# Optimization experiments

Measured on AMD Instinct MI355X. Metric: run time of the kernel, lower is better.

The kernel has to match this reference:

```python
import jax, jax.numpy as jnp
import numpy as np

N_SRC0, N_DST0 = 200000, 50000
N_DST1 = 10000
D_IN, D_HID = 128, 128


def _sage_mean(h, src, dst, n_dst, W_self, b_self, W_neigh, b_neigh, act):
    # gather messages from src nodes, mean-aggregate per dst node
    msg = h[src]                                             # [E, D]
    agg = jax.ops.segment_sum(msg, dst, num_segments=n_dst)  # [n_dst, D]
    deg = jax.ops.segment_sum(jnp.ones(dst.shape, h.dtype), dst, num_segments=n_dst)
    h_neigh = agg / jnp.maximum(deg, 1.0)[:, None]
    # DGL block convention: dst nodes are the first n_dst src nodes
    rst = h[:n_dst] @ W_self + b_self + h_neigh @ W_neigh + b_neigh
    return jax.nn.relu(rst) if act else rst


def setup_inputs() -> dict:
    key = jax.random.key(0)
    ks = jax.random.split(key, 12)
    s = 1.0 / np.sqrt(D_HID)
    return {
        "features": jax.random.normal(ks[0], (N_SRC0, D_IN), jnp.float32),
        "src0": jax.random.randint(ks[1], (800000,), 0, N_SRC0),
        "dst0": jax.random.randint(ks[2], (800000,), 0, N_DST0),
        "src1": jax.random.randint(ks[3], (160000,), 0, N_DST0),
        "dst1": jax.random.randint(ks[4], (160000,), 0, N_DST1),
        "W_init": jax.random.uniform(ks[5], (D_IN, D_HID), jnp.float32, -s, s),
        "b_init": jax.random.uniform(ks[6], (D_HID,), jnp.float32, -s, s),
        "W_self": jax.random.uniform(ks[7], (D_HID, D_HID), jnp.float32, -s, s),
        "b_self": jax.random.uniform(ks[8], (D_HID,), jnp.float32, -s, s),
        "W_neigh": jax.random.uniform(ks[9], (D_HID, D_HID), jnp.float32, -s, s),
        "b_neigh": jax.random.uniform(ks[10], (D_HID,), jnp.float32, -s, s),
    }


def reference(features, src0, dst0, src1, dst1, W_init, b_init, W_self, b_self, W_neigh, b_neigh):
    # fc_init + activation
    h = jax.nn.relu(features @ W_init + b_init)              # [N_SRC0, D_HID]
    # block 0 (act_flag True), dropout p=0.0 is identity
    h = _sage_mean(h, src0, dst0, N_DST0, W_self, b_self, W_neigh, b_neigh, act=True)
    # block 1 (last block: act_flag False)
    h = _sage_mean(h, src1, dst1, N_DST1, W_self, b_self, W_neigh, b_neigh, act=False)
    return jnp.squeeze(h, axis=1) if h.shape[1] == 1 else h  # h.squeeze(1) no-op for D_HID>1
```

## Files before the change

### kernel.cpp

```cpp
#include <hip/hip_runtime.h>
#include <stdint.h>
#include <stddef.h>


#define DIM 128
constexpr int N_SRC0 = 200000;
constexpr int N_DST0 = 50000;
constexpr int N_DST1 = 10000;
constexpr int E0 = 800000;
constexpr int E1 = 160000;
constexpr int MAXDEG = 64;

constexpr int FC_BLOCKS = 1024;
constexpr int PLACE_BLOCKS = 1024;

typedef __attribute__((ext_vector_type(8))) short bf16x8;
typedef __attribute__((ext_vector_type(4))) float f32x4;

__device__ __forceinline__ uint16_t f2bf(float f) {
  union { float f; uint32_t u; } v; v.f = f;
  return (uint16_t)((v.u + 0x7FFFu + ((v.u >> 16) & 1u)) >> 16);
}
__device__ __forceinline__ float bf2f(uint16_t h) {
  union { uint32_t u; float f; } v; v.u = ((uint32_t)h) << 16;
  return v.f;
}

__global__ __launch_bounds__(512) void prep_w_kernel(
    const float* __restrict__ W0, const float* __restrict__ W1,
    const float* __restrict__ W2, uint16_t* __restrict__ Wf,
    int* __restrict__ cnt, int ncnt) {
  int gid = blockIdx.x * 512 + threadIdx.x;
  if (gid < 3 * 16384) {
    int m = gid >> 14, idx = gid & 16383;
    const float* W = m == 0 ? W0 : (m == 1 ? W1 : W2);
    int j = idx & 7, lane = (idx >> 3) & 63, nt = (idx >> 9) & 7, kc = idx >> 12;
    int k = kc * 32 + (lane >> 4) * 8 + j;
    int n = nt * 16 + (lane & 15);
    Wf[gid] = f2bf(W[k * DIM + n]);
  }
  int z = gid - 3 * 16384;
  if (z >= 0 && z < ncnt) cnt[z] = 0;
}

__global__ __launch_bounds__(256, 4) void place_fc_kernel(
    const int* __restrict__ src0, const int* __restrict__ dst0,
    const int* __restrict__ src1, const int* __restrict__ dst1,
    int* __restrict__ cnt0, int* __restrict__ cnt1,
    int* __restrict__ eslot0, int* __restrict__ eslot1,
    const float* __restrict__ feat, const uint16_t* __restrict__ Wf,
    const float* __restrict__ bias, uint16_t* __restrict__ hout) {
  __shared__ __align__(16) float tile[2][4096];

  if ((blockIdx.x & 1) == 0) {
    int pb = blockIdx.x >> 1;
    int part = pb & 7;
    int bpp  = PLACE_BLOCKS >> 3;
    int bidx = pb >> 3;
    const int4* s04 = (const int4*)src0;
    const int4* d04 = (const int4*)dst0;
    const int4* s14 = (const int4*)src1;
    const int4* d14 = (const int4*)dst1;

    int lo = part * (N_DST0 / 8), hi = lo + (N_DST0 / 8);
    for (int i = bidx * 256 + threadIdx.x; i < E0 / 4; i += bpp * 256) {
      int4 d = d04[i]; int4 s = s04[i];
      if (d.x >= lo && d.x < hi) { int p = atomicAdd(&cnt0[d.x], 1); if (p < MAXDEG) eslot0[(size_t)d.x * MAXDEG + p] = s.x; }
      if (d.y >= lo && d.y < hi) { int p = atomicAdd(&cnt0[d.y], 1); if (p < MAXDEG) eslot0[(size_t)d.y * MAXDEG + p] = s.y; }
      if (d.z >= lo && d.z < hi) { int p = atomicAdd(&cnt0[d.z], 1); if (p < MAXDEG) eslot0[(size_t)d.z * MAXDEG + p] = s.z; }
      if (d.w >= lo && d.w < hi) { int p = atomicAdd(&cnt0[d.w], 1); if (p < MAXDEG) eslot0[(size_t)d.w * MAXDEG + p] = s.w; }
    }
    int lo1 = part * (N_DST1 / 8), hi1 = lo1 + (N_DST1 / 8);
    for (int i = bidx * 256 + threadIdx.x; i < E1 / 4; i += bpp * 256) {
      int4 d = d14[i]; int4 s = s14[i];
      if (d.x >= lo1 && d.x < hi1) { int p = atomicAdd(&cnt1[d.x], 1); if (p < MAXDEG) eslot1[(size_t)d.x * MAXDEG + p] = s.x; }
      if (d.y >= lo1 && d.y < hi1) { int p = atomicAdd(&cnt1[d.y], 1); if (p < MAXDEG) eslot1[(size_t)d.y * MAXDEG + p] = s.y; }
      if (d.z >= lo1 && d.z < hi1) { int p = atomicAdd(&cnt1[d.z], 1); if (p < MAXDEG) eslot1[(size_t)d.z * MAXDEG + p] = s.z; }
      if (d.w >= lo1 && d.w < hi1) { int p = atomicAdd(&cnt1[d.w], 1); if (p < MAXDEG) eslot1[(size_t)d.w * MAXDEG + p] = s.w; }
    }
    return;
  }

  const int tid = threadIdx.x;
  const int w = tid >> 6, lane = tid & 63;
  const int q = lane >> 4, m16 = lane & 15;
  const int sl = w >> 1, nh = w & 1;

  bf16x8 wv[4][4];
#pragma unroll
  for (int kc = 0; kc < 4; kc++)
#pragma unroll
    for (int j = 0; j < 4; j++)
      wv[kc][j] = *(const bf16x8*)&Wf[((size_t)((kc * 8 + nh * 4 + j) * 64 + lane)) * 8];

  float bv[4];
#pragma unroll
  for (int j = 0; j < 4; j++) bv[j] = bias[(nh * 4 + j) * 16 + m16];

  const int ntiles = N_SRC0 / 32;

  const int lrow0 = w * 8 + (lane >> 5);
  auto stage = [&](int t, int buf) {
#pragma unroll
    for (int i = 0; i < 4; i++) {
      int row = lrow0 + i * 2;
      int g = (lane & 31) ^ (row & 7);
      const float* gs = feat + (size_t)t * 4096 + row * 128 + g * 4;
      float* ld = &tile[buf][w * 1024 + i * 256];
      __builtin_amdgcn_global_load_lds(
          (const __attribute__((address_space(1))) uint32_t*)gs,
          (__attribute__((address_space(3))) uint32_t*)ld,
          16, 0, 0);
    }
  };

  int t = blockIdx.x >> 1;
  int cur = 0;
  if (t < ntiles) stage(t, 0);
  __syncthreads();

  const int trow = sl * 16 + m16;
  const int sw = trow & 7;

  while (t < ntiles) {
    int tn = t + FC_BLOCKS;
    if (tn < ntiles) stage(tn, cur ^ 1);

    f32x4 acc[4];
#pragma unroll
    for (int j = 0; j < 4; j++) acc[j] = (f32x4){0.f, 0.f, 0.f, 0.f};

    const char* rb = (const char*)&tile[cur][0] + trow * 512;
#pragma unroll
    for (int kc = 0; kc < 4; kc++) {
      int g0 = kc * 8 + q * 2;
      float4 x0 = *(const float4*)(rb + ((g0    ) ^ sw) * 16);
      float4 x1 = *(const float4*)(rb + ((g0 + 1) ^ sw) * 16);
      bf16x8 a;
      a[0] = (short)f2bf(x0.x); a[1] = (short)f2bf(x0.y);
      a[2] = (short)f2bf(x0.z); a[3] = (short)f2bf(x0.w);
      a[4] = (short)f2bf(x1.x); a[5] = (short)f2bf(x1.y);
      a[6] = (short)f2bf(x1.z); a[7] = (short)f2bf(x1.w);
#pragma unroll
      for (int j = 0; j < 4; j++)
        acc[j] = __builtin_amdgcn_mfma_f32_16x16x32_bf16(a, wv[kc][j], acc[j], 0, 0, 0);
    }

    int rowb = t * 32 + sl * 16 + q * 4;
#pragma unroll
    for (int j = 0; j < 4; j++)
#pragma unroll
      for (int r = 0; r < 4; r++) {
        float v = fmaxf(acc[j][r] + bv[j], 0.f);
        hout[(size_t)(rowb + r) * DIM + (nh * 4 + j) * 16 + m16] = f2bf(v);
      }

    __syncthreads();
    cur ^= 1;
    t = tn;
  }
}

__global__ __launch_bounds__(256) void agg_kernel(
    const int* __restrict__ eslot, const int* __restrict__ deg,
    const uint16_t* __restrict__ hsrc, uint16_t* __restrict__ hout, int n_dst) {
  int d = (blockIdx.x * 256 + threadIdx.x) >> 6;
  int lane = threadIdx.x & 63;
  if (d >= n_dst) return;
  const int* sl = eslot + (size_t)d * MAXDEG;
  int dg = deg[d];
  int dgc = dg < MAXDEG ? dg : MAXDEG;
  int qr = lane >> 4;
  int c  = lane & 15;

  float a0 = 0.f, a1 = 0.f, a2 = 0.f, a3 = 0.f;
  float a4 = 0.f, a5 = 0.f, a6 = 0.f, a7 = 0.f;

#define ACC4(P)                                                          \
  a0 += bf2f((uint16_t)(P).x); a1 += bf2f((uint16_t)((P).x >> 16));      \
  a2 += bf2f((uint16_t)(P).y); a3 += bf2f((uint16_t)((P).y >> 16));      \
  a4 += bf2f((uint16_t)(P).z); a5 += bf2f((uint16_t)((P).z >> 16));      \
  a6 += bf2f((uint16_t)(P).w); a7 += bf2f((uint16_t)((P).w >> 16));

  int e = 0;
  for (; e + 8 <= dgc; e += 8) {
    int s0 = sl[e + qr];
    int s1 = sl[e + 4 + qr];
    uint4 p0 = *(const uint4*)(hsrc + (size_t)s0 * DIM + c * 8);
    uint4 p1 = *(const uint4*)(hsrc + (size_t)s1 * DIM + c * 8);
    ACC4(p0); ACC4(p1);
  }
  for (; e + 4 <= dgc; e += 4) {
    int s0 = sl[e + qr];
    uint4 p0 = *(const uint4*)(hsrc + (size_t)s0 * DIM + c * 8);
    ACC4(p0);
  }
  int rem = dgc - e;
  if (qr < rem) {
    int s0 = sl[e + qr];
    uint4 p0 = *(const uint4*)(hsrc + (size_t)s0 * DIM + c * 8);
    ACC4(p0);
  }
#undef ACC4

  a0 += __shfl_xor(a0, 16); a0 += __shfl_xor(a0, 32);
  a1 += __shfl_xor(a1, 16); a1 += __shfl_xor(a1, 32);
  a2 += __shfl_xor(a2, 16); a2 += __shfl_xor(a2, 32);
  a3 += __shfl_xor(a3, 16); a3 += __shfl_xor(a3, 32);
  a4 += __shfl_xor(a4, 16); a4 += __shfl_xor(a4, 32);
  a5 += __shfl_xor(a5, 16); a5 += __shfl_xor(a5, 32);
  a6 += __shfl_xor(a6, 16); a6 += __shfl_xor(a6, 32);
  a7 += __shfl_xor(a7, 16); a7 += __shfl_xor(a7, 32);

  if (qr == 0) {
    float inv = 1.f / fmaxf((float)dg, 1.f);
    uint4 o;
    o.x = (uint32_t)f2bf(a0 * inv) | ((uint32_t)f2bf(a1 * inv) << 16);
    o.y = (uint32_t)f2bf(a2 * inv) | ((uint32_t)f2bf(a3 * inv) << 16);
    o.z = (uint32_t)f2bf(a4 * inv) | ((uint32_t)f2bf(a5 * inv) << 16);
    o.w = (uint32_t)f2bf(a6 * inv) | ((uint32_t)f2bf(a7 * inv) << 16);
    *(uint4*)(hout + (size_t)d * DIM + c * 8) = o;
  }
}

template <bool ACT, bool OUT_BF16>
__global__ __launch_bounds__(256) void sage_kernel(
    const uint16_t* __restrict__ hself, const uint16_t* __restrict__ hneigh,
    const uint16_t* __restrict__ WfS, const uint16_t* __restrict__ WfN,
    const float* __restrict__ bS, const float* __restrict__ bN,
    void* __restrict__ outp, int n_dst) {
  __shared__ uint16_t wS[16384];
  __shared__ uint16_t wN[16384];
  {
    const uint4* gS = (const uint4*)WfS;
    const uint4* gN = (const uint4*)WfN;
    uint4* sS = (uint4*)wS;
    uint4* sN = (uint4*)wN;
    for (int i = threadIdx.x; i < 2048; i += 256) { sS[i] = gS[i]; sN[i] = gN[i]; }
  }
  __syncthreads();

  int wave = (blockIdx.x * 256 + threadIdx.x) >> 6;
  int nwaves = (gridDim.x * 256) >> 6;
  int lane = threadIdx.x & 63;
  int q = lane >> 4, m16 = lane & 15;

  float bv[8];
#pragma unroll
  for (int nt = 0; nt < 8; nt++)
    bv[nt] = bS[nt * 16 + m16] + bN[nt * 16 + m16];

  const int nstrips = n_dst / 16;
  int s = wave;
  bf16x8 XS[4], XN[4];
  if (s < nstrips) {
    size_t ro = (size_t)(s * 16 + m16) * DIM + q * 8;
#pragma unroll
    for (int kc = 0; kc < 4; kc++) {
      XS[kc] = *(const bf16x8*)(hself + ro + kc * 32);
      XN[kc] = *(const bf16x8*)(hneigh + ro + kc * 32);
    }
  }

  while (s < nstrips) {
    int sn = s + nwaves;
    bf16x8 YS[4], YN[4];
    if (sn < nstrips) {
      size_t ro = (size_t)(sn * 16 + m16) * DIM + q * 8;
#pragma unroll
      for (int kc = 0; kc < 4; kc++) {
        YS[kc] = *(const bf16x8*)(hself + ro + kc * 32);
        YN[kc] = *(const bf16x8*)(hneigh + ro + kc * 32);
      }
    }

    f32x4 acc[8];
#pragma unroll
    for (int nt = 0; nt < 8; nt++) acc[nt] = (f32x4){0.f, 0.f, 0.f, 0.f};

#pragma unroll
    for (int kc = 0; kc < 4; kc++) {
#pragma unroll
      for (int nt = 0; nt < 8; nt++) {
        size_t fo = (size_t)((kc * 8 + nt) * 64 + lane) * 8;
        bf16x8 ws = *(const bf16x8*)&wS[fo];
        bf16x8 wn = *(const bf16x8*)&wN[fo];
        acc[nt] = __builtin_amdgcn_mfma_f32_16x16x32_bf16(XS[kc], ws, acc[nt], 0, 0, 0);
        acc[nt] = __builtin_amdgcn_mfma_f32_16x16x32_bf16(XN[kc], wn, acc[nt], 0, 0, 0);
      }
    }

    int m0 = s * 16;
#pragma unroll
    for (int nt = 0; nt < 8; nt++)
#pragma unroll
      for (int r = 0; r < 4; r++) {
        float v = acc[nt][r] + bv[nt];
        if (ACT) v = fmaxf(v, 0.f);
        size_t o = (size_t)(m0 + q * 4 + r) * DIM + nt * 16 + m16;
        if (OUT_BF16) ((uint16_t*)outp)[o] = f2bf(v);
        else          ((float*)outp)[o] = v;
      }

#pragma unroll
    for (int i = 0; i < 4; i++) { XS[i] = YS[i]; XN[i] = YN[i]; }
    s = sn;
  }
}

extern "C" void kernel_launch(void* const* d_in, const int* in_sizes, int n_in,
                              void* d_out, int out_size, void* d_ws, size_t ws_size,
                              hipStream_t stream) {
  const float* feat   = (const float*)d_in[0];
  const int* src0     = (const int*)d_in[1];
  const int* dst0     = (const int*)d_in[2];
  const int* src1     = (const int*)d_in[3];
  const int* dst1     = (const int*)d_in[4];
  const float* W_init = (const float*)d_in[5];
  const float* b_init = (const float*)d_in[6];
  const float* W_self = (const float*)d_in[7];
  const float* b_self = (const float*)d_in[8];
  const float* W_neigh= (const float*)d_in[9];
  const float* b_neigh= (const float*)d_in[10];

  char* ws = (char*)d_ws;
  uint16_t* h     = (uint16_t*)(ws + 0);
  uint16_t* h1    = (uint16_t*)(ws + 51200000);
  uint16_t* hn    = (uint16_t*)(ws + 64000000);
  int*      cnt0  = (int*)(ws + 76800000);
  int*      cnt1  = (int*)(ws + 77000000);
  int*      eslot0= (int*)(ws + 77040000);
  int*      eslot1= (int*)(ws + 89840000);
  uint16_t* WfI   = (uint16_t*)(ws + 92400000);
  uint16_t* WfS   = WfI + 16384;
  uint16_t* WfN   = WfS + 16384;

  prep_w_kernel<<<214, 512, 0, stream>>>(W_init, W_self, W_neigh, WfI, cnt0, 60000);

  place_fc_kernel<<<PLACE_BLOCKS + FC_BLOCKS, 256, 0, stream>>>(
      src0, dst0, src1, dst1, cnt0, cnt1, eslot0, eslot1,
      feat, WfI, b_init, h);

  agg_kernel<<<N_DST0 / 4, 256, 0, stream>>>(eslot0, cnt0, h, hn, N_DST0);
  sage_kernel<true, true><<<512, 256, 0, stream>>>(h, hn, WfS, WfN, b_self, b_neigh,
                                                   h1, N_DST0);

  agg_kernel<<<N_DST1 / 4, 256, 0, stream>>>(eslot1, cnt1, h1, hn, N_DST1);
  sage_kernel<false, false><<<160, 256, 0, stream>>>(h1, hn, WfS, WfN, b_self, b_neigh,
                                                     d_out, N_DST1);
}
```

Baseline: 270.6 us.

## Fold weight prep into fused kernels, drop LDS staging in fc_init, retune grids

Removes the separate prep_w kernel. W_init is now converted to bf16 MFMA layout in LDS by each fc block, W_self/W_neigh are converted by extra blocks in the first agg kernel, and counters are zeroed with hipMemsetAsync. The fc_init path now has each wave load a 16-row strip straight from global into registers, with no double-buffered LDS tiles, and computes all 8 N-tiles per wave. Place blocks are halved to a 1:2 ratio and the sage grid sizes change. Each fc block now repeats the W_init conversion, and the fc loads lose the async LDS prefetch.

```diff
diff --git a/kernel.cpp b/kernel.cpp
--- a/kernel.cpp
+++ b/kernel.cpp
@@ -11,8 +11,9 @@
 constexpr int E1 = 160000;
 constexpr int MAXDEG = 64;
 
+constexpr int PLACE_BLOCKS = 512;
 constexpr int FC_BLOCKS = 1024;
-constexpr int PLACE_BLOCKS = 1024;
+constexpr int PF_GRID = PLACE_BLOCKS + FC_BLOCKS;
 
 typedef __attribute__((ext_vector_type(8))) short bf16x8;
 typedef __attribute__((ext_vector_type(4))) float f32x4;
@@ -26,34 +27,17 @@
   return v.f;
 }
 
-__global__ __launch_bounds__(512) void prep_w_kernel(
-    const float* __restrict__ W0, const float* __restrict__ W1,
-    const float* __restrict__ W2, uint16_t* __restrict__ Wf,
-    int* __restrict__ cnt, int ncnt) {
-  int gid = blockIdx.x * 512 + threadIdx.x;
-  if (gid < 3 * 16384) {
-    int m = gid >> 14, idx = gid & 16383;
-    const float* W = m == 0 ? W0 : (m == 1 ? W1 : W2);
-    int j = idx & 7, lane = (idx >> 3) & 63, nt = (idx >> 9) & 7, kc = idx >> 12;
-    int k = kc * 32 + (lane >> 4) * 8 + j;
-    int n = nt * 16 + (lane & 15);
-    Wf[gid] = f2bf(W[k * DIM + n]);
-  }
-  int z = gid - 3 * 16384;
-  if (z >= 0 && z < ncnt) cnt[z] = 0;
-}
-
-__global__ __launch_bounds__(256, 4) void place_fc_kernel(
+__global__ __launch_bounds__(256) void place_fc_kernel(
     const int* __restrict__ src0, const int* __restrict__ dst0,
     const int* __restrict__ src1, const int* __restrict__ dst1,
     int* __restrict__ cnt0, int* __restrict__ cnt1,
     int* __restrict__ eslot0, int* __restrict__ eslot1,
-    const float* __restrict__ feat, const uint16_t* __restrict__ Wf,
+    const float* __restrict__ feat, const float* __restrict__ W_init,
     const float* __restrict__ bias, uint16_t* __restrict__ hout) {
-  __shared__ __align__(16) float tile[2][4096];
-
-  if ((blockIdx.x & 1) == 0) {
-    int pb = blockIdx.x >> 1;
+  __shared__ uint16_t wlds[16384];
+
+  if (blockIdx.x % 3 == 0) {
+    int pb = blockIdx.x / 3;
     int part = pb & 7;
     int bpp  = PLACE_BLOCKS >> 3;
     int bidx = pb >> 3;
@@ -81,89 +65,86 @@
     return;
   }
 
-  const int tid = threadIdx.x;
-  const int w = tid >> 6, lane = tid & 63;
+  for (int i = threadIdx.x; i < 16384; i += 256) {
+    int k = i >> 7, n = i & 127;
+    int off = (((k >> 5) * 8 + (n >> 4)) * 64 + ((k >> 3) & 3) * 16 + (n & 15)) * 8 + (k & 7);
+    wlds[off] = f2bf(W_init[i]);
+  }
+  __syncthreads();
+
+  int fcb = blockIdx.x - (blockIdx.x / 3 + 1);
+  const int lane = threadIdx.x & 63;
   const int q = lane >> 4, m16 = lane & 15;
-  const int sl = w >> 1, nh = w & 1;
-
-  bf16x8 wv[4][4];
-#pragma unroll
-  for (int kc = 0; kc < 4; kc++)
-#pragma unroll
-    for (int j = 0; j < 4; j++)
-      wv[kc][j] = *(const bf16x8*)&Wf[((size_t)((kc * 8 + nh * 4 + j) * 64 + lane)) * 8];
-
-  float bv[4];
-#pragma unroll
-  for (int j = 0; j < 4; j++) bv[j] = bias[(nh * 4 + j) * 16 + m16];
-
-  const int ntiles = N_SRC0 / 32;
-
-  const int lrow0 = w * 8 + (lane >> 5);
-  auto stage = [&](int t, int buf) {
-#pragma unroll
-    for (int i = 0; i < 4; i++) {
-      int row = lrow0 + i * 2;
-      int g = (lane & 31) ^ (row & 7);
-      const float* gs = feat + (size_t)t * 4096 + row * 128 + g * 4;
-      float* ld = &tile[buf][w * 1024 + i * 256];
-      __builtin_amdgcn_global_load_lds(
-          (const __attribute__((address_space(1))) uint32_t*)gs,
-          (__attribute__((address_space(3))) uint32_t*)ld,
-          16, 0, 0);
-    }
-  };
-
-  int t = blockIdx.x >> 1;
-  int cur = 0;
-  if (t < ntiles) stage(t, 0);
-  __syncthreads();
-
-  const int trow = sl * 16 + m16;
-  const int sw = trow & 7;
-
-  while (t < ntiles) {
-    int tn = t + FC_BLOCKS;
-    if (tn < ntiles) stage(tn, cur ^ 1);
-
-    f32x4 acc[4];
-#pragma unroll
-    for (int j = 0; j < 4; j++) acc[j] = (f32x4){0.f, 0.f, 0.f, 0.f};
-
-    const char* rb = (const char*)&tile[cur][0] + trow * 512;
+
+  float bv[8];
+#pragma unroll
+  for (int nt = 0; nt < 8; nt++) bv[nt] = bias[nt * 16 + m16];
+
+  const int nstrips = N_SRC0 / 16;
+  const int nw = FC_BLOCKS * 4;
+  int wave = fcb * 4 + (threadIdx.x >> 6);
+
+  for (int s = wave; s < nstrips; s += nw) {
+    const float* fr = feat + (size_t)(s * 16 + m16) * DIM + q * 8;
+    float4 x0[4], x1[4];
 #pragma unroll
     for (int kc = 0; kc < 4; kc++) {
-      int g0 = kc * 8 + q * 2;
-      float4 x0 = *(const float4*)(rb + ((g0    ) ^ sw) * 16);
-      float4 x1 = *(const float4*)(rb + ((g0 + 1) ^ sw) * 16);
-      bf16x8 a;
-      a[0] = (short)f2bf(x0.x); a[1] = (short)f2bf(x0.y);
-      a[2] = (short)f2bf(x0.z); a[3] = (short)f2bf(x0.w);
-      a[4] = (short)f2bf(x1.x); a[5] = (short)f2bf(x1.y);
-      a[6] = (short)f2bf(x1.z); a[7] = (short)f2bf(x1.w);
-#pragma unroll
-      for (int j = 0; j < 4; j++)
-        acc[j] = __builtin_amdgcn_mfma_f32_16x16x32_bf16(a, wv[kc][j], acc[j], 0, 0, 0);
-    }
-
-    int rowb = t * 32 + sl * 16 + q * 4;
-#pragma unroll
-    for (int j = 0; j < 4; j++)
+      x0[kc] = *(const float4*)(fr + kc * 32);
+      x1[kc] = *(const float4*)(fr + kc * 32 + 4);
+    }
+    bf16x8 a[4];
+#pragma unroll
+    for (int kc = 0; kc < 4; kc++) {
+      a[kc][0] = (short)f2bf(x0[kc].x); a[kc][1] = (short)f2bf(x0[kc].y);
+      a[kc][2] = (short)f2bf(x0[kc].z); a[kc][3] = (short)f2bf(x0[kc].w);
+      a[kc][4] = (short)f2bf(x1[kc].x); a[kc][5] = (short)f2bf(x1[kc].y);
+      a[kc][6] = (short)f2bf(x1[kc].z); a[kc][7] = (short)f2bf(x1[kc].w);
+    }
+
+    f32x4 acc[8];
+#pragma unroll
+    for (int nt = 0; nt < 8; nt++) acc[nt] = (f32x4){0.f, 0.f, 0.f, 0.f};
+
+#pragma unroll
+    for (int kc = 0; kc < 4; kc++)
+#pragma unroll
+      for (int nt = 0; nt < 8; nt++) {
+        bf16x8 wv = *(const bf16x8*)&wlds[((size_t)((kc * 8 + nt) * 64 + lane)) * 8];
+        acc[nt] = __builtin_amdgcn_mfma_f32_16x16x32_bf16(a[kc], wv, acc[nt], 0, 0, 0);
+      }
+
+    int rowb = s * 16 + q * 4;
+#pragma unroll
+    for (int nt = 0; nt < 8; nt++)
 #pragma unroll
       for (int r = 0; r < 4; r++) {
-        float v = fmaxf(acc[j][r] + bv[j], 0.f);
-        hout[(size_t)(rowb + r) * DIM + (nh * 4 + j) * 16 + m16] = f2bf(v);
-      }
-
-    __syncthreads();
-    cur ^= 1;
-    t = tn;
+        float v = fmaxf(acc[nt][r] + bv[nt], 0.f);
+        hout[(size_t)(rowb + r) * DIM + nt * 16 + m16] = f2bf(v);
+      }
   }
 }
 
 __global__ __launch_bounds__(256) void agg_kernel(
     const int* __restrict__ eslot, const int* __restrict__ deg,
-    const uint16_t* __restrict__ hsrc, uint16_t* __restrict__ hout, int n_dst) {
+    const uint16_t* __restrict__ hsrc, uint16_t* __restrict__ hout, int n_dst,
+    const float* __restrict__ WS_src, const float* __restrict__ WN_src,
+    uint16_t* __restrict__ Wf_out) {
+  int nagg = n_dst >> 2;
+  if (blockIdx.x >= nagg) {
+    int pid = (blockIdx.x - nagg) * 256 + threadIdx.x;
+#pragma unroll
+    for (int u = 0; u < 4; u++) {
+      int gid = pid * 4 + u;
+      int m = gid >> 14, idx = gid & 16383;
+      const float* W = m ? WN_src : WS_src;
+      int j = idx & 7, lane = (idx >> 3) & 63, nt = (idx >> 9) & 7, kc = idx >> 12;
+      int k = kc * 32 + (lane >> 4) * 8 + j;
+      int n = nt * 16 + (lane & 15);
+      Wf_out[gid] = f2bf(W[k * DIM + n]);
+    }
+    return;
+  }
+
   int d = (blockIdx.x * 256 + threadIdx.x) >> 6;
   int lane = threadIdx.x & 63;
   if (d >= n_dst) return;
@@ -335,17 +316,19 @@
   uint16_t* WfS   = WfI + 16384;
   uint16_t* WfN   = WfS + 16384;
 
-  prep_w_kernel<<<214, 512, 0, stream>>>(W_init, W_self, W_neigh, WfI, cnt0, 60000);
-
-  place_fc_kernel<<<PLACE_BLOCKS + FC_BLOCKS, 256, 0, stream>>>(
+  hipMemsetAsync(ws + 76800000, 0, 240000, stream);
+
+  place_fc_kernel<<<PF_GRID, 256, 0, stream>>>(
       src0, dst0, src1, dst1, cnt0, cnt1, eslot0, eslot1,
-      feat, WfI, b_init, h);
-
-  agg_kernel<<<N_DST0 / 4, 256, 0, stream>>>(eslot0, cnt0, h, hn, N_DST0);
-  sage_kernel<true, true><<<512, 256, 0, stream>>>(h, hn, WfS, WfN, b_self, b_neigh,
+      feat, W_init, b_init, h);
+
+  agg_kernel<<<N_DST0 / 4 + 32, 256, 0, stream>>>(eslot0, cnt0, h, hn, N_DST0,
+                                                  W_self, W_neigh, WfS);
+  sage_kernel<true, true><<<782, 256, 0, stream>>>(h, hn, WfS, WfN, b_self, b_neigh,
                                                    h1, N_DST0);
 
-  agg_kernel<<<N_DST1 / 4, 256, 0, stream>>>(eslot1, cnt1, h1, hn, N_DST1);
-  sage_kernel<false, false><<<160, 256, 0, stream>>>(h1, hn, WfS, WfN, b_self, b_neigh,
+  agg_kernel<<<N_DST1 / 4, 256, 0, stream>>>(eslot1, cnt1, h1, hn, N_DST1,
+                                             nullptr, nullptr, nullptr);
+  sage_kernel<false, false><<<157, 256, 0, stream>>>(h1, hn, WfS, WfN, b_self, b_neigh,
                                                      d_out, N_DST1);
 }
```

Result: slower. 335.0 us (+23.8%).

## Drop weight-prep kernel, convert weights inline, unroll gather, retune sage grids

Applied to the files above, without the earlier changes.

Removes the separate weight-prep kernel. Counters are now zeroed with hipMemsetAsync, the FC blocks convert W_init to bf16 directly from fp32 in registers, and the W_self/W_neigh swizzle is folded into 32 extra blocks of the first aggregation launch. The aggregation loop gains a 16-edge unrolled step for more memory-level parallelism, and the sage kernels' grid sizes change to 782 and 157 blocks. Each FC block now does strided scalar fp32 loads of W_init instead of vector loads of pre-swizzled bf16.

```diff
diff --git a/kernel.cpp b/kernel.cpp
--- a/kernel.cpp
+++ b/kernel.cpp
@@ -26,29 +26,12 @@
   return v.f;
 }
 
-__global__ __launch_bounds__(512) void prep_w_kernel(
-    const float* __restrict__ W0, const float* __restrict__ W1,
-    const float* __restrict__ W2, uint16_t* __restrict__ Wf,
-    int* __restrict__ cnt, int ncnt) {
-  int gid = blockIdx.x * 512 + threadIdx.x;
-  if (gid < 3 * 16384) {
-    int m = gid >> 14, idx = gid & 16383;
-    const float* W = m == 0 ? W0 : (m == 1 ? W1 : W2);
-    int j = idx & 7, lane = (idx >> 3) & 63, nt = (idx >> 9) & 7, kc = idx >> 12;
-    int k = kc * 32 + (lane >> 4) * 8 + j;
-    int n = nt * 16 + (lane & 15);
-    Wf[gid] = f2bf(W[k * DIM + n]);
-  }
-  int z = gid - 3 * 16384;
-  if (z >= 0 && z < ncnt) cnt[z] = 0;
-}
-
 __global__ __launch_bounds__(256, 4) void place_fc_kernel(
     const int* __restrict__ src0, const int* __restrict__ dst0,
     const int* __restrict__ src1, const int* __restrict__ dst1,
     int* __restrict__ cnt0, int* __restrict__ cnt1,
     int* __restrict__ eslot0, int* __restrict__ eslot1,
-    const float* __restrict__ feat, const uint16_t* __restrict__ Wf,
+    const float* __restrict__ feat, const float* __restrict__ W_init,
     const float* __restrict__ bias, uint16_t* __restrict__ hout) {
   __shared__ __align__(16) float tile[2][4096];
 
@@ -90,8 +73,11 @@
 #pragma unroll
   for (int kc = 0; kc < 4; kc++)
 #pragma unroll
-    for (int j = 0; j < 4; j++)
-      wv[kc][j] = *(const bf16x8*)&Wf[((size_t)((kc * 8 + nh * 4 + j) * 64 + lane)) * 8];
+    for (int jj = 0; jj < 4; jj++)
+#pragma unroll
+      for (int j = 0; j < 8; j++)
+        wv[kc][jj][j] = (short)f2bf(
+            W_init[(size_t)(kc * 32 + (lane >> 4) * 8 + j) * DIM + (nh * 4 + jj) * 16 + m16]);
 
   float bv[4];
 #pragma unroll
@@ -163,7 +149,25 @@
 
 __global__ __launch_bounds__(256) void agg_kernel(
     const int* __restrict__ eslot, const int* __restrict__ deg,
-    const uint16_t* __restrict__ hsrc, uint16_t* __restrict__ hout, int n_dst) {
+    const uint16_t* __restrict__ hsrc, uint16_t* __restrict__ hout, int n_dst,
+    const float* __restrict__ WS_src, const float* __restrict__ WN_src,
+    uint16_t* __restrict__ Wf_out) {
+  int nagg = n_dst >> 2;
+  if (blockIdx.x >= nagg) {
+    int pid = (blockIdx.x - nagg) * 256 + threadIdx.x;
+#pragma unroll
+    for (int u = 0; u < 4; u++) {
+      int gid = pid * 4 + u;
+      int m = gid >> 14, idx = gid & 16383;
+      const float* W = m ? WN_src : WS_src;
+      int j = idx & 7, lane = (idx >> 3) & 63, nt = (idx >> 9) & 7, kc = idx >> 12;
+      int k = kc * 32 + (lane >> 4) * 8 + j;
+      int n = nt * 16 + (lane & 15);
+      Wf_out[gid] = f2bf(W[k * DIM + n]);
+    }
+    return;
+  }
+
   int d = (blockIdx.x * 256 + threadIdx.x) >> 6;
   int lane = threadIdx.x & 63;
   if (d >= n_dst) return;
@@ -183,6 +187,17 @@
   a6 += bf2f((uint16_t)(P).w); a7 += bf2f((uint16_t)((P).w >> 16));
 
   int e = 0;
+  for (; e + 16 <= dgc; e += 16) {
+    int s0 = sl[e + qr];
+    int s1 = sl[e + 4 + qr];
+    int s2 = sl[e + 8 + qr];
+    int s3 = sl[e + 12 + qr];
+    uint4 p0 = *(const uint4*)(hsrc + (size_t)s0 * DIM + c * 8);
+    uint4 p1 = *(const uint4*)(hsrc + (size_t)s1 * DIM + c * 8);
+    uint4 p2 = *(const uint4*)(hsrc + (size_t)s2 * DIM + c * 8);
+    uint4 p3 = *(const uint4*)(hsrc + (size_t)s3 * DIM + c * 8);
+    ACC4(p0); ACC4(p1); ACC4(p2); ACC4(p3);
+  }
   for (; e + 8 <= dgc; e += 8) {
     int s0 = sl[e + qr];
     int s1 = sl[e + 4 + qr];
@@ -335,17 +350,19 @@
   uint16_t* WfS   = WfI + 16384;
   uint16_t* WfN   = WfS + 16384;
 
-  prep_w_kernel<<<214, 512, 0, stream>>>(W_init, W_self, W_neigh, WfI, cnt0, 60000);
+  hipMemsetAsync(ws + 76800000, 0, 240000, stream);
 
   place_fc_kernel<<<PLACE_BLOCKS + FC_BLOCKS, 256, 0, stream>>>(
       src0, dst0, src1, dst1, cnt0, cnt1, eslot0, eslot1,
-      feat, WfI, b_init, h);
-
-  agg_kernel<<<N_DST0 / 4, 256, 0, stream>>>(eslot0, cnt0, h, hn, N_DST0);
-  sage_kernel<true, true><<<512, 256, 0, stream>>>(h, hn, WfS, WfN, b_self, b_neigh,
+      feat, W_init, b_init, h);
+
+  agg_kernel<<<N_DST0 / 4 + 32, 256, 0, stream>>>(eslot0, cnt0, h, hn, N_DST0,
+                                                  W_self, W_neigh, WfS);
+  sage_kernel<true, true><<<782, 256, 0, stream>>>(h, hn, WfS, WfN, b_self, b_neigh,
                                                    h1, N_DST0);
 
-  agg_kernel<<<N_DST1 / 4, 256, 0, stream>>>(eslot1, cnt1, h1, hn, N_DST1);
-  sage_kernel<false, false><<<160, 256, 0, stream>>>(h1, hn, WfS, WfN, b_self, b_neigh,
+  agg_kernel<<<N_DST1 / 4, 256, 0, stream>>>(eslot1, cnt1, h1, hn, N_DST1,
+                                             nullptr, nullptr, nullptr);
+  sage_kernel<false, false><<<157, 256, 0, stream>>>(h1, hn, WfS, WfN, b_self, b_neigh,
                                                      d_out, N_DST1);
 }
```

New measurement: 303.9 us. +12.3%, slower.
